# Optimization experiments

Measured on AMD Instinct MI355X. Metric: run time of the kernel, lower is better.

## Reference

```python
import jax, jax.numpy as jnp
import numpy as np

MLP_CHANNELS = 128
MLP_KERNEL = 5


def setup_inputs() -> dict:
    key = jax.random.key(0)
    k1, k2 = jax.random.split(key)
    b, c, h, w = 16, MLP_CHANNELS, 128, 128
    num_w = MLP_KERNEL ** 2 * c + c  # 3328
    inp = jax.random.normal(k1, (b, c, h, w), dtype=jnp.float32)
    # mimic ini_weights_ scaling: conv weights ~ N(0, 6/(k^2+c)), bias ~ N(0, 1/c)
    weights = jax.random.normal(k2, (b, num_w), dtype=jnp.float32)
    off = MLP_KERNEL ** 2 * c
    scale = jnp.concatenate([
        jnp.full((off,), np.sqrt(6.0 / (MLP_KERNEL ** 2 + c)), dtype=jnp.float32),
        jnp.full((c,), np.sqrt(1.0 / c), dtype=jnp.float32),
    ])
    weights = weights * scale[None, :]
    return {"input": inp, "weights": weights}


def reference(input, weights):
    b, c, h, w = input.shape
    k = MLP_KERNEL
    off = k * k * c
    # per-sample depthwise filters [b, c, 1, k, k] and biases [b, c]
    wk = weights[:, :off].reshape(b, c, 1, k, k)
    bias = weights[:, off:off + c]

    def dwconv(x, wt):
        # x: [c,h,w], wt: [c,1,k,k]; depthwise conv via feature_group_count=c
        return jax.lax.conv_general_dilated(
            x[None], wt, window_strides=(1, 1), padding='SAME',
            dimension_numbers=('NCHW', 'OIHW', 'NCHW'),
            feature_group_count=c)[0]

    out = jax.vmap(dwconv)(input, wk)          # [b,c,h,w]
    out = out + bias[:, :, None, None]          # fused bias
    return jax.nn.silu(out)                     # act
```

## Files before the change

### kernel.cpp

```cpp
#include <hip/hip_runtime.h>
#include <math.h>

#define C_CH 128
#define HW 128
#define KK 5
#define NW (KK*KK*C_CH + C_CH)
#define RPT 16

__global__ __launch_bounds__(256, 6) void hyperconv_dw_silu(
    const float* __restrict__ inp, const float* __restrict__ wts,
    float* __restrict__ out)
{
    const int tid = threadIdx.x;
    const int c   = blockIdx.x;
    const int b   = blockIdx.y;

    const float* wt = wts + (size_t)b * NW;
    float wk[25];
#pragma unroll
    for (int j = 0; j < 25; ++j) wk[j] = wt[c * 25 + j];
    const float bias = wt[KK * KK * C_CH + c];

    const float* plane  = inp + ((size_t)(b * C_CH + c)) * (HW * HW);
    float*       oplane = out + ((size_t)(b * C_CH + c)) * (HW * HW);

    const int colg = tid & 31;
    const int rowg = tid >> 5;
    const int r0   = rowg * RPT;
    const int xb   = colg * 4;
    const int lcb  = (colg == 0)  ? 0   : (xb - 4);
    const int rcb  = (colg == 31) ? 120 : (xb + 4);

    float w[5][8];

    auto load_row = [&](int ir, float* wr) {
        const int irc = (ir < 0) ? 0 : ((ir > 127) ? 127 : ir);
        const float* row = plane + irc * HW;
        const float4 xl = *(const float4*)(row + lcb);
        const float4 xm = *(const float4*)(row + xb);
        const float4 xr = *(const float4*)(row + rcb);
        const bool vz = (ir < 0) | (ir > 127);
        const bool lz = vz | (colg == 0);
        const bool rz = vz | (colg == 31);
        wr[0] = lz ? 0.f : xl.z;
        wr[1] = lz ? 0.f : xl.w;
        wr[2] = vz ? 0.f : xm.x;
        wr[3] = vz ? 0.f : xm.y;
        wr[4] = vz ? 0.f : xm.z;
        wr[5] = vz ? 0.f : xm.w;
        wr[6] = rz ? 0.f : xr.x;
        wr[7] = rz ? 0.f : xr.y;
    };

#pragma unroll
    for (int i = 0; i < 4; ++i) load_row(r0 - 2 + i, w[i]);

#pragma unroll
    for (int s = 0; s < RPT; ++s) {
        load_row(r0 + s + 2, w[(s + 4) % 5]);

        float acc[4] = {bias, bias, bias, bias};
#pragma unroll
        for (int kh = 0; kh < 5; ++kh) {
            const float* wr = w[(s + kh) % 5];
#pragma unroll
            for (int oc = 0; oc < 4; ++oc)
#pragma unroll
                for (int kw = 0; kw < 5; ++kw)
                    acc[oc] = fmaf(wk[kh * 5 + kw], wr[oc + kw], acc[oc]);
        }

        float4 o;
        o.x = acc[0] * __builtin_amdgcn_rcpf(1.0f + __expf(-acc[0]));
        o.y = acc[1] * __builtin_amdgcn_rcpf(1.0f + __expf(-acc[1]));
        o.z = acc[2] * __builtin_amdgcn_rcpf(1.0f + __expf(-acc[2]));
        o.w = acc[3] * __builtin_amdgcn_rcpf(1.0f + __expf(-acc[3]));
        *(float4*)(oplane + (size_t)(r0 + s) * HW + xb) = o;
    }
}

extern "C" void kernel_launch(void* const* d_in, const int* in_sizes, int n_in,
                              void* d_out, int out_size, void* d_ws, size_t ws_size,
                              hipStream_t stream) {
    const float* inp = (const float*)d_in[0];
    const float* wts = (const float*)d_in[1];
    float* out = (float*)d_out;

    const int batch = in_sizes[1] / NW;
    dim3 grid(C_CH, batch);
    hyperconv_dw_silu<<<grid, 256, 0, stream>>>(inp, wts, out);
}
```

Before: 246.2 us.

## Split each plane across two blocks and scatter input rows into accumulators

Each block now covers half a channel plane, so each thread handles 8 output rows and the grid doubles to 2×C×B blocks. Input rows are loaded once each and scattered into all the output-row accumulators they touch, instead of keeping a rotating 5-row window. Outputs are written with nontemporal stores. The aim is more parallelism and streaming writes that bypass the cache, at the cost of more halo reloads (12 input rows per 8 output rows versus 20 per 16), more accumulator registers, and a lower launch-bounds occupancy hint.

Result: no change. 245.9 us (-0.1%).

```diff
diff --git a/kernel.cpp b/kernel.cpp
--- a/kernel.cpp
+++ b/kernel.cpp
@@ -5,15 +5,19 @@
 #define HW 128
 #define KK 5
 #define NW (KK*KK*C_CH + C_CH)
-#define RPT 16
+#define TR 8
+#define IR (TR + 4)
 
-__global__ __launch_bounds__(256, 6) void hyperconv_dw_silu(
+typedef float __attribute__((ext_vector_type(4))) floatx4;
+
+__global__ __launch_bounds__(256, 4) void hyperconv_dw_silu(
     const float* __restrict__ inp, const float* __restrict__ wts,
     float* __restrict__ out)
 {
-    const int tid = threadIdx.x;
-    const int c   = blockIdx.x;
-    const int b   = blockIdx.y;
+    const int tid  = threadIdx.x;
+    const int half = blockIdx.x;
+    const int c    = blockIdx.y;
+    const int b    = blockIdx.z;
 
     const float* wt = wts + (size_t)b * NW;
     float wk[25];
@@ -26,14 +30,20 @@
 
     const int colg = tid & 31;
     const int rowg = tid >> 5;
-    const int r0   = rowg * RPT;
+    const int r0   = half * 64 + rowg * TR;
     const int xb   = colg * 4;
     const int lcb  = (colg == 0)  ? 0   : (xb - 4);
     const int rcb  = (colg == 31) ? 120 : (xb + 4);
 
-    float w[5][8];
+    float acc[TR][4];
+#pragma unroll
+    for (int i = 0; i < TR; ++i)
+#pragma unroll
+        for (int j = 0; j < 4; ++j) acc[i][j] = bias;
 
-    auto load_row = [&](int ir, float* wr) {
+#pragma unroll
+    for (int r = 0; r < IR; ++r) {
+        const int ir  = r0 - 2 + r;
         const int irc = (ir < 0) ? 0 : ((ir > 127) ? 127 : ir);
         const float* row = plane + irc * HW;
         const float4 xl = *(const float4*)(row + lcb);
@@ -42,40 +52,39 @@
         const bool vz = (ir < 0) | (ir > 127);
         const bool lz = vz | (colg == 0);
         const bool rz = vz | (colg == 31);
-        wr[0] = lz ? 0.f : xl.z;
-        wr[1] = lz ? 0.f : xl.w;
-        wr[2] = vz ? 0.f : xm.x;
-        wr[3] = vz ? 0.f : xm.y;
-        wr[4] = vz ? 0.f : xm.z;
-        wr[5] = vz ? 0.f : xm.w;
-        wr[6] = rz ? 0.f : xr.x;
-        wr[7] = rz ? 0.f : xr.y;
-    };
+
+        float x[8];
+        x[0] = lz ? 0.f : xl.z;
+        x[1] = lz ? 0.f : xl.w;
+        x[2] = vz ? 0.f : xm.x;
+        x[3] = vz ? 0.f : xm.y;
+        x[4] = vz ? 0.f : xm.z;
+        x[5] = vz ? 0.f : xm.w;
+        x[6] = rz ? 0.f : xr.x;
+        x[7] = rz ? 0.f : xr.y;
 
 #pragma unroll
-    for (int i = 0; i < 4; ++i) load_row(r0 - 2 + i, w[i]);
-
-#pragma unroll
-    for (int s = 0; s < RPT; ++s) {
-        load_row(r0 + s + 2, w[(s + 4) % 5]);
-
-        float acc[4] = {bias, bias, bias, bias};
-#pragma unroll
-        for (int kh = 0; kh < 5; ++kh) {
-            const float* wr = w[(s + kh) % 5];
+        for (int orow = 0; orow < TR; ++orow) {
+            const int kh = r - orow;
+            if (kh < 0 || kh > 4) continue;
 #pragma unroll
             for (int oc = 0; oc < 4; ++oc)
 #pragma unroll
                 for (int kw = 0; kw < 5; ++kw)
-                    acc[oc] = fmaf(wk[kh * 5 + kw], wr[oc + kw], acc[oc]);
+                    acc[orow][oc] = fmaf(wk[kh * 5 + kw], x[oc + kw], acc[orow][oc]);
         }
+    }
 
-        float4 o;
-        o.x = acc[0] * __builtin_amdgcn_rcpf(1.0f + __expf(-acc[0]));
-        o.y = acc[1] * __builtin_amdgcn_rcpf(1.0f + __expf(-acc[1]));
-        o.z = acc[2] * __builtin_amdgcn_rcpf(1.0f + __expf(-acc[2]));
-        o.w = acc[3] * __builtin_amdgcn_rcpf(1.0f + __expf(-acc[3]));
-        *(float4*)(oplane + (size_t)(r0 + s) * HW + xb) = o;
+#pragma unroll
+    for (int orow = 0; orow < TR; ++orow) {
+        const float v0 = acc[orow][0], v1 = acc[orow][1];
+        const float v2 = acc[orow][2], v3 = acc[orow][3];
+        floatx4 o;
+        o.x = v0 * __builtin_amdgcn_rcpf(1.0f + __expf(-v0));
+        o.y = v1 * __builtin_amdgcn_rcpf(1.0f + __expf(-v1));
+        o.z = v2 * __builtin_amdgcn_rcpf(1.0f + __expf(-v2));
+        o.w = v3 * __builtin_amdgcn_rcpf(1.0f + __expf(-v3));
+        __builtin_nontemporal_store(o, (floatx4*)(oplane + (size_t)(r0 + orow) * HW + xb));
     }
 }
 
@@ -87,6 +96,6 @@
     float* out = (float*)d_out;
 
     const int batch = in_sizes[1] / NW;
-    dim3 grid(C_CH, batch);
+    dim3 grid(2, C_CH, batch);
     hyperconv_dw_silu<<<grid, 256, 0, stream>>>(inp, wts, out);
 }
```
